# Kernel tuning notes

Hardware: AMD Instinct MI355X
Metric: run time of the kernel (lower is better)

The kernel has to match this reference:

```python
import jax, jax.numpy as jnp
import numpy as np


def setup_inputs() -> dict:
    key = jax.random.key(0)
    ks = jax.random.split(key, 8)
    B, L, E, U = 32, 2048, 1024, 1024
    s = 0.02
    return {
        "dec_hidden": jax.random.normal(ks[0], (B, E), jnp.float32),
        "enc_output": jax.random.normal(ks[1], (B, L, E), jnp.float32),
        "prev_coverage": jax.random.uniform(ks[2], (B, L, 1), jnp.float32),
        "Ws_k": jax.random.normal(ks[3], (E, U), jnp.float32) * s,
        "Ws_b": jnp.zeros((U,), jnp.float32),
        "Wh_k": jax.random.normal(ks[4], (E, U), jnp.float32) * s,
        "Wh_b": jnp.zeros((U,), jnp.float32),
        "Wc_k": jax.random.normal(ks[5], (1, U), jnp.float32) * s,
        "Wc_b": jnp.zeros((U,), jnp.float32),
        "V_k": jax.random.normal(ks[6], (U, 1), jnp.float32) * s,
        "V_b": jnp.zeros((1,), jnp.float32),
        "enc_pad_mask": jnp.ones((B, L), jnp.int32),
        "use_coverage": 1,
    }


def reference(dec_hidden, enc_output, prev_coverage, Ws_k, Ws_b, Wh_k, Wh_b,
              Wc_k, Wc_b, V_k, V_b, enc_pad_mask, use_coverage):
    # projections: [B,L,U] + [B,1,U] (+ [B,L,U] coverage term)
    pre = jnp.einsum('ble,eu->blu', enc_output, Ws_k) + Ws_b \
        + (dec_hidden @ Wh_k + Wh_b)[:, None, :]
    if use_coverage:
        pre = pre + (prev_coverage @ Wc_k + Wc_b)
    score = jnp.tanh(pre) @ V_k + V_b              # [B, L, 1]
    mask = enc_pad_mask.astype(score.dtype)        # [B, L]
    masked_score = (score[..., 0] * mask)[..., None]  # [B, L, 1]
    attention_weights = jax.nn.softmax(masked_score, axis=1)
    coverage = attention_weights + prev_coverage if use_coverage else attention_weights
    context_vector = jnp.sum(attention_weights * enc_output, axis=1)  # [B, E]
    return (context_vector, attention_weights, coverage)
```

## Files before the change

kernel.cpp:

```cpp
#include <hip/hip_runtime.h>
#include <hip/hip_bf16.h>
#include <math.h>

typedef float f32x4 __attribute__((ext_vector_type(4)));
typedef short short8 __attribute__((ext_vector_type(8)));
typedef unsigned short u16x8 __attribute__((ext_vector_type(8)));

static __device__ __forceinline__ unsigned short f2bf(float f) {
    unsigned u = __builtin_bit_cast(unsigned, f);
    unsigned r = (u + 0x7FFFu + ((u >> 16) & 1u)) >> 16;
    return (unsigned short)r;
}
static __device__ __forceinline__ float bf2f(unsigned short h) {
    unsigned u = ((unsigned)h) << 16;
    return __builtin_bit_cast(float, u);
}
static __device__ __forceinline__ float fast_tanh(float x) {
    float ax = fminf(fmaxf(x, -9.f), 9.f);
    float e = __expf(2.f * ax);
    return 1.f - 2.f / (e + 1.f);
}

#define GLD16(g, l) __builtin_amdgcn_global_load_lds(                        \
    (const __attribute__((address_space(1))) void*)(g),                      \
    (__attribute__((address_space(3))) void*)(l), 16, 0, 0)

__global__ __launch_bounds__(256) void prep_kernel(
    const float* __restrict__ enc, unsigned short* __restrict__ encB,
    const float* __restrict__ ws, unsigned short* __restrict__ wst,
    const float* __restrict__ dh, const float* __restrict__ whk,
    float* __restrict__ base_part)
{
    __shared__ unsigned short tile[64][65];
    __shared__ float dS[128];
    const int bid = blockIdx.x, tid = threadIdx.x;

    if (bid < 16384) {
        const size_t base0 = (size_t)bid * 4096;
#pragma unroll
        for (int i = 0; i < 4; i++) {
            size_t g = base0 + (size_t)i * 1024 + tid * 4;
            f32x4 v = *(const f32x4*)(enc + g);
            ushort4 w;
            w.x = f2bf(v.x); w.y = f2bf(v.y); w.z = f2bf(v.z); w.w = f2bf(v.w);
            *(ushort4*)(encB + g) = w;
        }
    } else if (bid < 16640) {
        const int b2 = bid - 16384;
        const int e0 = (b2 & 15) * 64, u0 = (b2 >> 4) * 64;
#pragma unroll
        for (int i = 0; i < 16; i++) {
            int idx = i * 256 + tid;
            int r = idx >> 6, c = idx & 63;
            tile[r][c] = f2bf(ws[(size_t)(e0 + r) * 1024 + u0 + c]);
        }
        __syncthreads();
#pragma unroll
        for (int i = 0; i < 16; i++) {
            int idx = i * 256 + tid;
            int r = idx >> 6, c = idx & 63;
            wst[(size_t)(u0 + r) * 1024 + e0 + c] = tile[c][r];
        }
    } else {
        const int b3 = bid - 16640;
        const int b = b3 & 31, ec = b3 >> 5;
        const int e0 = ec * 128;
        if (tid < 128) dS[tid] = dh[b * 1024 + e0 + tid];
        __syncthreads();
        f32x4 acc = {0.f, 0.f, 0.f, 0.f};
#pragma unroll 4
        for (int e = 0; e < 128; e++)
            acc += dS[e] * *(const f32x4*)(whk + (size_t)(e0 + e) * 1024 + tid * 4);
        *(f32x4*)(base_part + (size_t)ec * 32768 + b * 1024 + tid * 4) = acc;
    }
}

#define BARRM() asm volatile("s_barrier" ::: "memory")
#define PRIO1() __builtin_amdgcn_s_setprio(1)
#define PRIO0() __builtin_amdgcn_s_setprio(0)
#define VMC6()  asm volatile("s_waitcnt vmcnt(6)" ::: "memory")
#define VMC4()  asm volatile("s_waitcnt vmcnt(4)" ::: "memory")
#define VMC0()  asm volatile("s_waitcnt vmcnt(0)" ::: "memory")

__global__ __launch_bounds__(512, 2) void score_gemm_8ph(
    const unsigned short* __restrict__ encB,
    const unsigned short* __restrict__ wst,
    const float* __restrict__ base_part,
    const float* __restrict__ cov,
    const float* __restrict__ wc,
    const float* __restrict__ vk,
    const float* __restrict__ wsb, const float* __restrict__ whb,
    const float* __restrict__ wcb,
    const int* __restrict__ ucov,
    float* __restrict__ score_part)
{
    __shared__ __align__(16) unsigned short As[2][16384];
    __shared__ __align__(16) unsigned short Bs[2][16384];

    const int tid = threadIdx.x;
    const int bid = blockIdx.x;
    const int sidx = bid >> 3;
    const int row_blk = (bid & 7) * 32 + (sidx >> 2);
    const int u_blk = sidx & 3;
    const int row0 = row_blk << 8;
    const int u0 = u_blk << 8;

    const int lane = tid & 63;
    const int wid  = tid >> 6;
    const int wm = wid >> 2, wn = wid & 3;
    const int l16 = lane & 15, quad = lane >> 4;

    const int k8 = (lane & 7) ^ (lane >> 3);
    unsigned offA[2][2], offB[2][2];
    int dstA[2][2], dstB[2][2];
#pragma unroll
    for (int g = 0; g < 2; g++) {
        const int uu = wid * 2 + g;
#pragma unroll
        for (int h = 0; h < 2; h++) {
            const int ra = ((uu & 8) << 4) + (h << 6) + ((uu & 7) << 3);
            const int rb = ((uu >> 2) << 6) + (h << 5) + ((uu & 3) << 3);
            dstA[g][h] = ra * 64 + lane * 8;
            dstB[g][h] = rb * 64 + lane * 8;
            offA[g][h] = (unsigned)(row0 + ra + (lane >> 3)) * 1024u + (unsigned)(k8 * 8);
            offB[g][h] = (unsigned)(u0 + rb + (lane >> 3)) * 1024u + (unsigned)(k8 * 8);
        }
    }

    const int aBase = (wm * 128 + l16) * 64;
    const int bBase = (wn * 64 + l16) * 64;
    const int ch0 = ((quad) ^ (l16 & 7)) * 8;
    const int ch1 = ((4 + quad) ^ (l16 & 7)) * 8;

#define STAGE_A(bf, h, kt) do {                                             \
    GLD16(encB + offA[0][h] + ((kt) << 6), &As[bf][dstA[0][h]]);            \
    GLD16(encB + offA[1][h] + ((kt) << 6), &As[bf][dstA[1][h]]); } while (0)
#define STAGE_B(bf, h, kt) do {                                             \
    GLD16(wst + offB[0][h] + ((kt) << 6), &Bs[bf][dstB[0][h]]);             \
    GLD16(wst + offB[1][h] + ((kt) << 6), &Bs[bf][dstB[1][h]]); } while (0)

    f32x4 acc[8][4] = {};
    short8 aF[4][2], bF0[2][2], bF1[2][2];

#define LOAD_AF(bf, r) do {                                                 \
    _Pragma("unroll")                                                       \
    for (int fi = 0; fi < 4; fi++) {                                        \
        aF[fi][0] = *(const short8*)&As[bf][aBase + (r)*4096 + fi*1024 + ch0]; \
        aF[fi][1] = *(const short8*)&As[bf][aBase + (r)*4096 + fi*1024 + ch1]; \
    } } while (0)
#define LOAD_BF(bf, c, BF) do {                                             \
    _Pragma("unroll")                                                       \
    for (int fj = 0; fj < 2; fj++) {                                        \
        BF[fj][0] = *(const short8*)&Bs[bf][bBase + (c)*2048 + fj*1024 + ch0]; \
        BF[fj][1] = *(const short8*)&Bs[bf][bBase + (c)*2048 + fj*1024 + ch1]; \
    } } while (0)
#define MFMA16(r, c, BF) do {                                               \
    _Pragma("unroll")                                                       \
    for (int ks = 0; ks < 2; ks++)                                          \
    _Pragma("unroll")                                                       \
    for (int fi = 0; fi < 4; fi++)                                          \
    _Pragma("unroll")                                                       \
    for (int fj = 0; fj < 2; fj++)                                          \
        acc[(r)*4+fi][(c)*2+fj] = __builtin_amdgcn_mfma_f32_16x16x32_bf16(  \
            aF[fi][ks], BF[fj][ks], acc[(r)*4+fi][(c)*2+fj], 0, 0, 0);      \
    } while (0)

    STAGE_A(0, 0, 0);
    STAGE_B(0, 0, 0);
    STAGE_B(0, 1, 0);
    STAGE_A(0, 1, 0);
    STAGE_A(1, 0, 1);
    STAGE_B(1, 0, 1);
    STAGE_B(1, 1, 1);
    VMC6();
    BARRM();

#pragma unroll 1
    for (int i = 0; i < 7; i++) {
        const int t1 = 2 * i + 1, t2 = 2 * i + 2, t3 = 2 * i + 3;
        LOAD_AF(0, 0); LOAD_BF(0, 0, bF0); LOAD_BF(0, 1, bF1);
        STAGE_A(1, 1, t1);
        PRIO1(); MFMA16(0, 0, bF0); MFMA16(0, 1, bF1); PRIO0();
        BARRM();
        LOAD_AF(0, 1);
        STAGE_A(0, 0, t2); STAGE_B(0, 0, t2);
        PRIO1(); MFMA16(1, 0, bF0); MFMA16(1, 1, bF1); PRIO0();
        VMC4();
        BARRM();
        LOAD_AF(1, 0); LOAD_BF(1, 0, bF0); LOAD_BF(1, 1, bF1);
        STAGE_B(0, 1, t2); STAGE_A(0, 1, t2);
        PRIO1(); MFMA16(0, 0, bF0); MFMA16(0, 1, bF1); PRIO0();
        BARRM();
        LOAD_AF(1, 1);
        STAGE_A(1, 0, t3); STAGE_B(1, 0, t3); STAGE_B(1, 1, t3);
        PRIO1(); MFMA16(1, 0, bF0); MFMA16(1, 1, bF1); PRIO0();
        VMC6();
        BARRM();
    }

    LOAD_AF(0, 0); LOAD_BF(0, 0, bF0); LOAD_BF(0, 1, bF1);
    STAGE_A(1, 1, 15);
    PRIO1(); MFMA16(0, 0, bF0); MFMA16(0, 1, bF1); PRIO0();
    BARRM();
    LOAD_AF(0, 1);
    PRIO1(); MFMA16(1, 0, bF0); MFMA16(1, 1, bF1); PRIO0();
    VMC0();
    BARRM();
    LOAD_AF(1, 0); LOAD_BF(1, 0, bF0); LOAD_BF(1, 1, bF1);
    PRIO1(); MFMA16(0, 0, bF0); MFMA16(0, 1, bF1); PRIO0();
    BARRM();
    LOAD_AF(1, 1);
    PRIO1(); MFMA16(1, 0, bF0); MFMA16(1, 1, bF1); PRIO0();

    const int use_cov = *ucov;
    const int b = row0 >> 11;
    float baseR[4], wcR[4], vvR[4];
#pragma unroll
    for (int cf = 0; cf < 4; cf++) {
        int u = u0 + wn * 64 + cf * 16 + l16;
        float s = wsb[u] + whb[u] + (use_cov ? wcb[u] : 0.f);
#pragma unroll
        for (int p = 0; p < 8; p++) s += base_part[p * 32768 + b * 1024 + u];
        baseR[cf] = s;
        wcR[cf] = use_cov ? wc[u] : 0.f;
        vvR[cf] = vk[u];
    }
    float* sred = (float*)&Bs[0][0];
#pragma unroll
    for (int rf = 0; rf < 8; rf++) {
        float part[4] = {0.f, 0.f, 0.f, 0.f};
#pragma unroll
        for (int j = 0; j < 4; j++) {
            int rl = wm * 128 + rf * 16 + quad * 4 + j;
            float cvv = use_cov ? cov[row0 + rl] : 0.f;
#pragma unroll
            for (int cf = 0; cf < 4; cf++) {
                float pre = acc[rf][cf][j] + baseR[cf] + cvv * wcR[cf];
                part[j] += fast_tanh(pre) * vvR[cf];
            }
        }
#pragma unroll
        for (int j = 0; j < 4; j++) {
            float v = part[j];
            v += __shfl_xor(v, 1);
            v += __shfl_xor(v, 2);
            v += __shfl_xor(v, 4);
            v += __shfl_xor(v, 8);
            if (l16 == 0) sred[wn * 256 + wm * 128 + rf * 16 + quad * 4 + j] = v;
        }
    }
    __syncthreads();
    if (tid < 256)
        score_part[(size_t)u_blk * 65536 + row0 + tid] =
            sred[tid] + sred[256 + tid] + sred[512 + tid] + sred[768 + tid];

#undef STAGE_A
#undef STAGE_B
#undef LOAD_AF
#undef LOAD_BF
#undef MFMA16
}

__global__ __launch_bounds__(1024) void softmax_kernel(
    const float* __restrict__ score_part, int nplanes,
    const float* __restrict__ vb,
    const int* __restrict__ mask, const float* __restrict__ cov,
    const int* __restrict__ ucov,
    float* __restrict__ attn_out, float* __restrict__ cov_out)
{
    __shared__ float redA[16], redB[16];
    __shared__ float bc0, bc1;
    const int b = blockIdx.x, tid = threadIdx.x;
    const int i0 = b * 2048 + tid, i1 = i0 + 1024;
    const float vbv = vb[0];
    const int uc = *ucov;

    float s0 = 0.f, s1 = 0.f;
    for (int p = 0; p < nplanes; p++) {
        s0 += score_part[(size_t)p * 65536 + i0];
        s1 += score_part[(size_t)p * 65536 + i1];
    }
    s0 = (s0 + vbv) * (float)mask[i0];
    s1 = (s1 + vbv) * (float)mask[i1];

    float m = fmaxf(s0, s1);
#pragma unroll
    for (int off = 1; off < 64; off <<= 1) m = fmaxf(m, __shfl_xor(m, off));
    if ((tid & 63) == 0) redA[tid >> 6] = m;
    __syncthreads();
    if (tid < 16) {
        float v = redA[tid];
#pragma unroll
        for (int off = 1; off < 16; off <<= 1) v = fmaxf(v, __shfl_xor(v, off));
        if (tid == 0) bc0 = v;
    }
    __syncthreads();
    const float M = bc0;

    float e0 = __expf(s0 - M), e1 = __expf(s1 - M);
    float s = e0 + e1;
#pragma unroll
    for (int off = 1; off < 64; off <<= 1) s += __shfl_xor(s, off);
    if ((tid & 63) == 0) redB[tid >> 6] = s;
    __syncthreads();
    if (tid < 16) {
        float v = redB[tid];
#pragma unroll
        for (int off = 1; off < 16; off <<= 1) v += __shfl_xor(v, off);
        if (tid == 0) bc1 = v;
    }
    __syncthreads();
    const float inv = 1.f / bc1;

    float a0 = e0 * inv, a1 = e1 * inv;
    attn_out[i0] = a0;
    attn_out[i1] = a1;
    cov_out[i0] = a0 + (uc ? cov[i0] : 0.f);
    cov_out[i1] = a1 + (uc ? cov[i1] : 0.f);
}

__global__ __launch_bounds__(256) void context_bf16(const unsigned short* __restrict__ encB,
                                                    const float* __restrict__ attn,
                                                    float* __restrict__ out_ctx) {
    __shared__ float aS[2048];
    __shared__ float red[4][64];
    const int b = blockIdx.x, ec = blockIdx.y, tid = threadIdx.x;
    const int e0 = ec * 64;
    for (int i = tid; i < 2048; i += 256) aS[i] = attn[b * 2048 + i];
    __syncthreads();
    const int es = (tid & 7) * 8;
    const int lo = tid >> 3;
    float acc[8] = {};
    for (int l = lo; l < 2048; l += 32) {
        u16x8 w = *(const u16x8*)(encB + (size_t)(b * 2048 + l) * 1024 + e0 + es);
        float a = aS[l];
#pragma unroll
        for (int j = 0; j < 8; j++) acc[j] = fmaf(a, bf2f(w[j]), acc[j]);
    }
#pragma unroll
    for (int j = 0; j < 8; j++) {
        float v = acc[j];
        v += __shfl_xor(v, 8);
        v += __shfl_xor(v, 16);
        v += __shfl_xor(v, 32);
        acc[j] = v;
    }
    const int wv = tid >> 6;
    if ((tid & 63) < 8) {
#pragma unroll
        for (int j = 0; j < 8; j++) red[wv][(tid & 7) * 8 + j] = acc[j];
    }
    __syncthreads();
    if (tid < 64)
        out_ctx[b * 1024 + e0 + tid] = red[0][tid] + red[1][tid] + red[2][tid] + red[3][tid];
}

#define BM 128
#define BN 128
#define BK 32
#define LDT 40
__global__ __launch_bounds__(256) void score_gemm_f32(
    const float* __restrict__ enc, const unsigned short* __restrict__ wst,
    const float* __restrict__ base_part, const float* __restrict__ cov,
    const float* __restrict__ wc, const float* __restrict__ vk,
    const float* __restrict__ wsb, const float* __restrict__ whb,
    const float* __restrict__ wcb,
    const int* __restrict__ ucov, float* __restrict__ score)
{
    __shared__ unsigned short As[BM * LDT];
    __shared__ unsigned short Bs[BN * LDT];
    __shared__ float covS[BM];
    __shared__ float baseS[BN], wcS[BN], vvS[BN];
    const int tid = threadIdx.x;
    const int row0 = blockIdx.x * BM, u0 = blockIdx.y * BN;
    const int b = row0 >> 11;
    const int use_cov = *ucov;
    if (tid < BM) covS[tid] = use_cov ? cov[row0 + tid] : 0.f;
    if (tid < BN) {
        int u = u0 + tid;
        float s = wsb[u] + whb[u] + (use_cov ? wcb[u] : 0.f);
#pragma unroll
        for (int p = 0; p < 8; p++) s += base_part[p * 32768 + b * 1024 + u];
        baseS[tid] = s;
        wcS[tid] = use_cov ? wc[u] : 0.f;
        vvS[tid] = vk[u];
    }
    const int lane = tid & 63, wid = tid >> 6;
    const int wm = wid >> 1, wn = wid & 1;
    const int l16 = lane & 15, quad = lane >> 4;
    f32x4 acc[4][4] = {};
    for (int k0 = 0; k0 < 1024; k0 += BK) {
        __syncthreads();
#pragma unroll
        for (int i = 0; i < 4; i++) {
            int f = i * 256 + tid;
            int r = f >> 3, c4 = f & 7;
            const float* p = enc + (size_t)(row0 + r) * 1024 + k0 + c4 * 4;
            ushort4 w;
            w.x = f2bf(p[0]); w.y = f2bf(p[1]); w.z = f2bf(p[2]); w.w = f2bf(p[3]);
            *(ushort4*)&As[r * LDT + c4 * 4] = w;
        }
#pragma unroll
        for (int i = 0; i < 2; i++) {
            int f = i * 256 + tid;
            int r = f >> 2, c8 = f & 3;
            uint4 w = *(const uint4*)(wst + (size_t)(u0 + r) * 1024 + k0 + c8 * 8);
            *(uint4*)&Bs[r * LDT + c8 * 8] = w;
        }
        __syncthreads();
        short8 a[4], bb[4];
#pragma unroll
        for (int t = 0; t < 4; t++) {
            a[t]  = *(const short8*)&As[(wm * 64 + t * 16 + l16) * LDT + quad * 8];
            bb[t] = *(const short8*)&Bs[(wn * 64 + t * 16 + l16) * LDT + quad * 8];
        }
#pragma unroll
        for (int i = 0; i < 4; i++)
#pragma unroll
            for (int j = 0; j < 4; j++)
                acc[i][j] = __builtin_amdgcn_mfma_f32_16x16x32_bf16(a[i], bb[j], acc[i][j], 0, 0, 0);
    }
#pragma unroll
    for (int i = 0; i < 4; i++) {
        float part[4] = {0.f, 0.f, 0.f, 0.f};
#pragma unroll
        for (int r = 0; r < 4; r++) {
            float cv = covS[wm * 64 + i * 16 + quad * 4 + r];
#pragma unroll
            for (int j = 0; j < 4; j++) {
                int ul = wn * 64 + j * 16 + l16;
                part[r] += fast_tanh(acc[i][j][r] + baseS[ul] + cv * wcS[ul]) * vvS[ul];
            }
        }
#pragma unroll
        for (int r = 0; r < 4; r++) {
            float v = part[r];
            v += __shfl_xor(v, 1);
            v += __shfl_xor(v, 2);
            v += __shfl_xor(v, 4);
            v += __shfl_xor(v, 8);
            if (l16 == 0)
                atomicAdd(&score[row0 + wm * 64 + i * 16 + quad * 4 + r], v);
        }
    }
}

__global__ __launch_bounds__(256) void context_f32(const float* __restrict__ enc,
                                                   const float* __restrict__ attn,
                                                   float* __restrict__ ctx) {
    __shared__ float aS[128];
    const int b = blockIdx.x, lc = blockIdx.y, tid = threadIdx.x;
    const int l0 = lc * 128;
    if (tid < 128) aS[tid] = attn[b * 2048 + l0 + tid];
    __syncthreads();
    const float* p = enc + ((size_t)(b * 2048 + l0)) * 1024 + tid * 4;
    f32x4 acc = {0.f, 0.f, 0.f, 0.f};
#pragma unroll 4
    for (int l = 0; l < 128; l++) acc += *(const f32x4*)(p + (size_t)l * 1024) * aS[l];
    float* o = ctx + b * 1024 + tid * 4;
    atomicAdd(o + 0, acc.x);
    atomicAdd(o + 1, acc.y);
    atomicAdd(o + 2, acc.z);
    atomicAdd(o + 3, acc.w);
}

__global__ __launch_bounds__(256) void prep2_kernel(
    const float* __restrict__ ws, unsigned short* __restrict__ wst,
    const float* __restrict__ dh, const float* __restrict__ whk,
    float* __restrict__ base_part)
{
    __shared__ unsigned short tile[64][65];
    __shared__ float dS[128];
    const int bid = blockIdx.x, tid = threadIdx.x;
    if (bid < 256) {
        const int e0 = (bid & 15) * 64, u0 = (bid >> 4) * 64;
#pragma unroll
        for (int i = 0; i < 16; i++) {
            int idx = i * 256 + tid;
            int r = idx >> 6, c = idx & 63;
            tile[r][c] = f2bf(ws[(size_t)(e0 + r) * 1024 + u0 + c]);
        }
        __syncthreads();
#pragma unroll
        for (int i = 0; i < 16; i++) {
            int idx = i * 256 + tid;
            int r = idx >> 6, c = idx & 63;
            wst[(size_t)(u0 + r) * 1024 + e0 + c] = tile[c][r];
        }
    } else {
        const int b3 = bid - 256;
        const int b = b3 & 31, ec = b3 >> 5;
        const int e0 = ec * 128;
        if (tid < 128) dS[tid] = dh[b * 1024 + e0 + tid];
        __syncthreads();
        f32x4 acc = {0.f, 0.f, 0.f, 0.f};
#pragma unroll 4
        for (int e = 0; e < 128; e++)
            acc += dS[e] * *(const f32x4*)(whk + (size_t)(e0 + e) * 1024 + tid * 4);
        *(f32x4*)(base_part + (size_t)ec * 32768 + b * 1024 + tid * 4) = acc;
    }
}

extern "C" void kernel_launch(void* const* d_in, const int* in_sizes, int n_in,
                              void* d_out, int out_size, void* d_ws, size_t ws_size,
                              hipStream_t stream) {
    const float* dec_hidden = (const float*)d_in[0];
    const float* enc        = (const float*)d_in[1];
    const float* prev_cov   = (const float*)d_in[2];
    const float* Ws_k       = (const float*)d_in[3];
    const float* Ws_b       = (const float*)d_in[4];
    const float* Wh_k       = (const float*)d_in[5];
    const float* Wh_b       = (const float*)d_in[6];
    const float* Wc_k       = (const float*)d_in[7];
    const float* Wc_b       = (const float*)d_in[8];
    const float* V_k        = (const float*)d_in[9];
    const float* V_b        = (const float*)d_in[10];
    const int*   mask       = (const int*)d_in[11];
    const int*   ucov       = (const int*)d_in[12];

    float* out_ctx  = (float*)d_out;
    float* out_attn = out_ctx + 32 * 1024;
    float* out_cov  = out_attn + 65536;

    char* ws = (char*)d_ws;
    unsigned short* wst = (unsigned short*)ws;
    float* base_part  = (float*)(ws + 2097152);
    float* score_part = (float*)(ws + 3145728);
    unsigned short* encB = (unsigned short*)(ws + 5242880);
    const size_t need_fast = 5242880 + (size_t)32 * 2048 * 1024 * 2;

    if (ws_size >= need_fast) {
        prep_kernel<<<16896, 256, 0, stream>>>(enc, encB, Ws_k, wst, dec_hidden, Wh_k, base_part);
        score_gemm_8ph<<<dim3(1024), dim3(512), 0, stream>>>(
            encB, wst, base_part, prev_cov, Wc_k, V_k, Ws_b, Wh_b, Wc_b, ucov, score_part);
        softmax_kernel<<<32, 1024, 0, stream>>>(score_part, 4, V_b, mask, prev_cov, ucov, out_attn, out_cov);
        context_bf16<<<dim3(32, 16), 256, 0, stream>>>(encB, out_attn, out_ctx);
    } else {
        hipMemsetAsync(score_part, 0, 65536 * sizeof(float), stream);
        hipMemsetAsync(out_ctx, 0, 32 * 1024 * sizeof(float), stream);
        prep2_kernel<<<512, 256, 0, stream>>>(Ws_k, wst, dec_hidden, Wh_k, base_part);
        score_gemm_f32<<<dim3(512, 8), 256, 0, stream>>>(
            enc, wst, base_part, prev_cov, Wc_k, V_k, Ws_b, Wh_b, Wc_b, ucov, score_part);
        softmax_kernel<<<32, 1024, 0, stream>>>(score_part, 1, V_b, mask, prev_cov, ucov, out_attn, out_cov);
        context_f32<<<dim3(32, 16), 256, 0, stream>>>(enc, out_attn, out_ctx);
    }
}
```

Measured before the change: 592.5 us.

## Prefetch LDS fragments one phase ahead in score GEMM and fuse softmax into context

Restructures the 8-phase MFMA GEMM loop so the A and B fragments for the next phase are read from LDS while the current phase's MFMAs run. It uses double-buffered register fragments (aFA/aFB, bfE/bfO), loads B once per k-tile, and adjusts the vmcnt waits to match. Separately, it drops the standalone softmax launch and has each context block recompute the softmax over the score planes. That removes one kernel launch and the attention round-trip through global memory, at the cost of 16x redundant softmax work per batch row and more register pressure in the GEMM.

```diff
diff --git a/kernel.cpp b/kernel.cpp
--- a/kernel.cpp
+++ b/kernel.cpp
@@ -78,7 +78,7 @@
 #define BARRM() asm volatile("s_barrier" ::: "memory")
 #define PRIO1() __builtin_amdgcn_s_setprio(1)
 #define PRIO0() __builtin_amdgcn_s_setprio(0)
-#define VMC6()  asm volatile("s_waitcnt vmcnt(6)" ::: "memory")
+#define VMC8()  asm volatile("s_waitcnt vmcnt(8)" ::: "memory")
 #define VMC4()  asm volatile("s_waitcnt vmcnt(4)" ::: "memory")
 #define VMC0()  asm volatile("s_waitcnt vmcnt(0)" ::: "memory")
 
@@ -140,77 +140,76 @@
     GLD16(wst + offB[1][h] + ((kt) << 6), &Bs[bf][dstB[1][h]]); } while (0)
 
     f32x4 acc[8][4] = {};
-    short8 aF[4][2], bF0[2][2], bF1[2][2];
-
-#define LOAD_AF(bf, r) do {                                                 \
+    short8 aFA[4][2], aFB[4][2];
+    short8 bfE[2][2][2], bfO[2][2][2];
+
+#define LOAD_A(bf, r, DST) do {                                             \
     _Pragma("unroll")                                                       \
     for (int fi = 0; fi < 4; fi++) {                                        \
-        aF[fi][0] = *(const short8*)&As[bf][aBase + (r)*4096 + fi*1024 + ch0]; \
-        aF[fi][1] = *(const short8*)&As[bf][aBase + (r)*4096 + fi*1024 + ch1]; \
+        DST[fi][0] = *(const short8*)&As[bf][aBase + (r)*4096 + fi*1024 + ch0]; \
+        DST[fi][1] = *(const short8*)&As[bf][aBase + (r)*4096 + fi*1024 + ch1]; \
     } } while (0)
-#define LOAD_BF(bf, c, BF) do {                                             \
+#define LOAD_B(bf, DST) do {                                                \
+    _Pragma("unroll")                                                       \
+    for (int c = 0; c < 2; c++)                                             \
     _Pragma("unroll")                                                       \
     for (int fj = 0; fj < 2; fj++) {                                        \
-        BF[fj][0] = *(const short8*)&Bs[bf][bBase + (c)*2048 + fj*1024 + ch0]; \
-        BF[fj][1] = *(const short8*)&Bs[bf][bBase + (c)*2048 + fj*1024 + ch1]; \
+        DST[c][fj][0] = *(const short8*)&Bs[bf][bBase + c*2048 + fj*1024 + ch0]; \
+        DST[c][fj][1] = *(const short8*)&Bs[bf][bBase + c*2048 + fj*1024 + ch1]; \
     } } while (0)
-#define MFMA16(r, c, BF) do {                                               \
+#define MFMA_ROW(r, AF, BF) do {                                            \
     _Pragma("unroll")                                                       \
     for (int ks = 0; ks < 2; ks++)                                          \
     _Pragma("unroll")                                                       \
     for (int fi = 0; fi < 4; fi++)                                          \
     _Pragma("unroll")                                                       \
+    for (int c = 0; c < 2; c++)                                             \
+    _Pragma("unroll")                                                       \
     for (int fj = 0; fj < 2; fj++)                                          \
-        acc[(r)*4+fi][(c)*2+fj] = __builtin_amdgcn_mfma_f32_16x16x32_bf16(  \
-            aF[fi][ks], BF[fj][ks], acc[(r)*4+fi][(c)*2+fj], 0, 0, 0);      \
+        acc[(r)*4+fi][c*2+fj] = __builtin_amdgcn_mfma_f32_16x16x32_bf16(    \
+            AF[fi][ks], BF[c][fj][ks], acc[(r)*4+fi][c*2+fj], 0, 0, 0);     \
     } while (0)
 
-    STAGE_A(0, 0, 0);
-    STAGE_B(0, 0, 0);
-    STAGE_B(0, 1, 0);
-    STAGE_A(0, 1, 0);
-    STAGE_A(1, 0, 1);
-    STAGE_B(1, 0, 1);
-    STAGE_B(1, 1, 1);
-    VMC6();
+    STAGE_A(0, 0, 0); STAGE_B(0, 0, 0); STAGE_B(0, 1, 0); STAGE_A(0, 1, 0);
+    STAGE_A(1, 0, 1); STAGE_B(1, 0, 1); STAGE_B(1, 1, 1); STAGE_A(1, 1, 1);
+    VMC8();
     BARRM();
+    LOAD_A(0, 0, aFA); LOAD_B(0, bfE);
 
 #pragma unroll 1
     for (int i = 0; i < 7; i++) {
-        const int t1 = 2 * i + 1, t2 = 2 * i + 2, t3 = 2 * i + 3;
-        LOAD_AF(0, 0); LOAD_BF(0, 0, bF0); LOAD_BF(0, 1, bF1);
-        STAGE_A(1, 1, t1);
-        PRIO1(); MFMA16(0, 0, bF0); MFMA16(0, 1, bF1); PRIO0();
-        BARRM();
-        LOAD_AF(0, 1);
+        const int t2 = 2 * i + 2, t3 = 2 * i + 3;
+        LOAD_A(0, 1, aFB);
         STAGE_A(0, 0, t2); STAGE_B(0, 0, t2);
-        PRIO1(); MFMA16(1, 0, bF0); MFMA16(1, 1, bF1); PRIO0();
+        PRIO1(); MFMA_ROW(0, aFA, bfE); PRIO0();
         VMC4();
         BARRM();
-        LOAD_AF(1, 0); LOAD_BF(1, 0, bF0); LOAD_BF(1, 1, bF1);
+        LOAD_A(1, 0, aFA); LOAD_B(1, bfO);
         STAGE_B(0, 1, t2); STAGE_A(0, 1, t2);
-        PRIO1(); MFMA16(0, 0, bF0); MFMA16(0, 1, bF1); PRIO0();
+        PRIO1(); MFMA_ROW(1, aFB, bfE); PRIO0();
         BARRM();
-        LOAD_AF(1, 1);
-        STAGE_A(1, 0, t3); STAGE_B(1, 0, t3); STAGE_B(1, 1, t3);
-        PRIO1(); MFMA16(1, 0, bF0); MFMA16(1, 1, bF1); PRIO0();
-        VMC6();
+        LOAD_A(1, 1, aFB);
+        STAGE_A(1, 0, t3); STAGE_B(1, 0, t3);
+        PRIO1(); MFMA_ROW(0, aFA, bfO); PRIO0();
+        VMC4();
         BARRM();
-    }
-
-    LOAD_AF(0, 0); LOAD_BF(0, 0, bF0); LOAD_BF(0, 1, bF1);
-    STAGE_A(1, 1, 15);
-    PRIO1(); MFMA16(0, 0, bF0); MFMA16(0, 1, bF1); PRIO0();
-    BARRM();
-    LOAD_AF(0, 1);
-    PRIO1(); MFMA16(1, 0, bF0); MFMA16(1, 1, bF1); PRIO0();
+        LOAD_A(0, 0, aFA); LOAD_B(0, bfE);
+        STAGE_B(1, 1, t3); STAGE_A(1, 1, t3);
+        PRIO1(); MFMA_ROW(1, aFB, bfO); PRIO0();
+        BARRM();
+    }
+
+    LOAD_A(0, 1, aFB);
+    PRIO1(); MFMA_ROW(0, aFA, bfE); PRIO0();
     VMC0();
     BARRM();
-    LOAD_AF(1, 0); LOAD_BF(1, 0, bF0); LOAD_BF(1, 1, bF1);
-    PRIO1(); MFMA16(0, 0, bF0); MFMA16(0, 1, bF1); PRIO0();
+    LOAD_A(1, 0, aFA); LOAD_B(1, bfO);
+    PRIO1(); MFMA_ROW(1, aFB, bfE); PRIO0();
     BARRM();
-    LOAD_AF(1, 1);
-    PRIO1(); MFMA16(1, 0, bF0); MFMA16(1, 1, bF1); PRIO0();
+    LOAD_A(1, 1, aFB);
+    PRIO1(); MFMA_ROW(0, aFA, bfO); PRIO0();
+    BARRM();
+    PRIO1(); MFMA_ROW(1, aFB, bfO); PRIO0();
 
     const int use_cov = *ucov;
     const int b = row0 >> 11;
@@ -256,9 +255,102 @@
 
 #undef STAGE_A
 #undef STAGE_B
-#undef LOAD_AF
-#undef LOAD_BF
-#undef MFMA16
+#undef LOAD_A
+#undef LOAD_B
+#undef MFMA_ROW
+}
+
+__global__ __launch_bounds__(256) void context_fused(
+    const unsigned short* __restrict__ encB,
+    const float* __restrict__ score_part, int nplanes,
+    const float* __restrict__ vb,
+    const int* __restrict__ mask, const float* __restrict__ cov,
+    const int* __restrict__ ucov,
+    float* __restrict__ attn_out, float* __restrict__ cov_out,
+    float* __restrict__ out_ctx)
+{
+    __shared__ float aS[2048];
+    __shared__ float red[4][64];
+    __shared__ float redM[4], redS[4];
+    const int b = blockIdx.x, ec = blockIdx.y, tid = threadIdx.x;
+    const int e0 = ec * 64;
+    const int wv = tid >> 6;
+    const float vbv = vb[0];
+    const int uc = *ucov;
+
+    const int l0 = tid * 8;
+    float sv[8] = {0.f, 0.f, 0.f, 0.f, 0.f, 0.f, 0.f, 0.f};
+    for (int p = 0; p < nplanes; p++) {
+        const float* sp = score_part + (size_t)p * 65536 + b * 2048 + l0;
+        f32x4 v0 = *(const f32x4*)sp;
+        f32x4 v1 = *(const f32x4*)(sp + 4);
+        sv[0] += v0.x; sv[1] += v0.y; sv[2] += v0.z; sv[3] += v0.w;
+        sv[4] += v1.x; sv[5] += v1.y; sv[6] += v1.z; sv[7] += v1.w;
+    }
+    int4 mk0 = *(const int4*)(mask + b * 2048 + l0);
+    int4 mk1 = *(const int4*)(mask + b * 2048 + l0 + 4);
+    sv[0] = (sv[0] + vbv) * (float)mk0.x;
+    sv[1] = (sv[1] + vbv) * (float)mk0.y;
+    sv[2] = (sv[2] + vbv) * (float)mk0.z;
+    sv[3] = (sv[3] + vbv) * (float)mk0.w;
+    sv[4] = (sv[4] + vbv) * (float)mk1.x;
+    sv[5] = (sv[5] + vbv) * (float)mk1.y;
+    sv[6] = (sv[6] + vbv) * (float)mk1.z;
+    sv[7] = (sv[7] + vbv) * (float)mk1.w;
+
+    float m = sv[0];
+#pragma unroll
+    for (int j = 1; j < 8; j++) m = fmaxf(m, sv[j]);
+#pragma unroll
+    for (int off = 1; off < 64; off <<= 1) m = fmaxf(m, __shfl_xor(m, off));
+    if ((tid & 63) == 0) redM[wv] = m;
+    __syncthreads();
+    const float M = fmaxf(fmaxf(redM[0], redM[1]), fmaxf(redM[2], redM[3]));
+
+    float e[8], s = 0.f;
+#pragma unroll
+    for (int j = 0; j < 8; j++) { e[j] = __expf(sv[j] - M); s += e[j]; }
+#pragma unroll
+    for (int off = 1; off < 64; off <<= 1) s += __shfl_xor(s, off);
+    if ((tid & 63) == 0) redS[wv] = s;
+    __syncthreads();
+    const float inv = 1.f / (redS[0] + redS[1] + redS[2] + redS[3]);
+
+#pragma unroll
+    for (int j = 0; j < 8; j++) {
+        float a = e[j] * inv;
+        aS[l0 + j] = a;
+        if (ec == 0) {
+            attn_out[b * 2048 + l0 + j] = a;
+            cov_out[b * 2048 + l0 + j] = a + (uc ? cov[b * 2048 + l0 + j] : 0.f);
+        }
+    }
+    __syncthreads();
+
+    const int es = (tid & 7) * 8;
+    const int lo = tid >> 3;
+    float acc[8] = {};
+    for (int l = lo; l < 2048; l += 32) {
+        u16x8 w = *(const u16x8*)(encB + (size_t)(b * 2048 + l) * 1024 + e0 + es);
+        float a = aS[l];
+#pragma unroll
+        for (int j = 0; j < 8; j++) acc[j] = fmaf(a, bf2f(w[j]), acc[j]);
+    }
+#pragma unroll
+    for (int j = 0; j < 8; j++) {
+        float v = acc[j];
+        v += __shfl_xor(v, 8);
+        v += __shfl_xor(v, 16);
+        v += __shfl_xor(v, 32);
+        acc[j] = v;
+    }
+    if ((tid & 63) < 8) {
+#pragma unroll
+        for (int j = 0; j < 8; j++) red[wv][(tid & 7) * 8 + j] = acc[j];
+    }
+    __syncthreads();
+    if (tid < 64)
+        out_ctx[b * 1024 + e0 + tid] = red[0][tid] + red[1][tid] + red[2][tid] + red[3][tid];
 }
 
 __global__ __launch_bounds__(1024) void softmax_kernel(
@@ -317,42 +409,6 @@
     attn_out[i1] = a1;
     cov_out[i0] = a0 + (uc ? cov[i0] : 0.f);
     cov_out[i1] = a1 + (uc ? cov[i1] : 0.f);
-}
-
-__global__ __launch_bounds__(256) void context_bf16(const unsigned short* __restrict__ encB,
-                                                    const float* __restrict__ attn,
-                                                    float* __restrict__ out_ctx) {
-    __shared__ float aS[2048];
-    __shared__ float red[4][64];
-    const int b = blockIdx.x, ec = blockIdx.y, tid = threadIdx.x;
-    const int e0 = ec * 64;
-    for (int i = tid; i < 2048; i += 256) aS[i] = attn[b * 2048 + i];
-    __syncthreads();
-    const int es = (tid & 7) * 8;
-    const int lo = tid >> 3;
-    float acc[8] = {};
-    for (int l = lo; l < 2048; l += 32) {
-        u16x8 w = *(const u16x8*)(encB + (size_t)(b * 2048 + l) * 1024 + e0 + es);
-        float a = aS[l];
-#pragma unroll
-        for (int j = 0; j < 8; j++) acc[j] = fmaf(a, bf2f(w[j]), acc[j]);
-    }
-#pragma unroll
-    for (int j = 0; j < 8; j++) {
-        float v = acc[j];
-        v += __shfl_xor(v, 8);
-        v += __shfl_xor(v, 16);
-        v += __shfl_xor(v, 32);
-        acc[j] = v;
-    }
-    const int wv = tid >> 6;
-    if ((tid & 63) < 8) {
-#pragma unroll
-        for (int j = 0; j < 8; j++) red[wv][(tid & 7) * 8 + j] = acc[j];
-    }
-    __syncthreads();
-    if (tid < 64)
-        out_ctx[b * 1024 + e0 + tid] = red[0][tid] + red[1][tid] + red[2][tid] + red[3][tid];
 }
 
 #define BM 128
@@ -533,8 +589,8 @@
         prep_kernel<<<16896, 256, 0, stream>>>(enc, encB, Ws_k, wst, dec_hidden, Wh_k, base_part);
         score_gemm_8ph<<<dim3(1024), dim3(512), 0, stream>>>(
             encB, wst, base_part, prev_cov, Wc_k, V_k, Ws_b, Wh_b, Wc_b, ucov, score_part);
-        softmax_kernel<<<32, 1024, 0, stream>>>(score_part, 4, V_b, mask, prev_cov, ucov, out_attn, out_cov);
-        context_bf16<<<dim3(32, 16), 256, 0, stream>>>(encB, out_attn, out_ctx);
+        context_fused<<<dim3(32, 16), 256, 0, stream>>>(
+            encB, score_part, 4, V_b, mask, prev_cov, ucov, out_attn, out_cov, out_ctx);
     } else {
         hipMemsetAsync(score_part, 0, 65536 * sizeof(float), stream);
         hipMemsetAsync(out_ctx, 0, 32 * 1024 * sizeof(float), stream);
```

After: 1.144 ms. 93.1% more time.

## Fuse softmax into context kernel and widen nontemporal bf16 conversion loads

Applied to the files above, without the earlier changes.

The separate softmax launch is removed. Each of the 16 context blocks per batch now recomputes the softmax over its batch row redundantly, and only the ec==0 blocks write attention and coverage. The context kernel goes from 256 to 512 threads. The enc fp32-to-bf16 conversion in prep now handles 8 elements per thread with nontemporal loads and 16-byte stores. The intent is to save a launch and a global round trip for the attention weights, at the cost of recomputing the softmax 16 times.

```diff
diff --git a/kernel.cpp b/kernel.cpp
--- a/kernel.cpp
+++ b/kernel.cpp
@@ -38,12 +38,14 @@
     if (bid < 16384) {
         const size_t base0 = (size_t)bid * 4096;
 #pragma unroll
-        for (int i = 0; i < 4; i++) {
-            size_t g = base0 + (size_t)i * 1024 + tid * 4;
-            f32x4 v = *(const f32x4*)(enc + g);
-            ushort4 w;
-            w.x = f2bf(v.x); w.y = f2bf(v.y); w.z = f2bf(v.z); w.w = f2bf(v.w);
-            *(ushort4*)(encB + g) = w;
+        for (int i = 0; i < 2; i++) {
+            size_t g = base0 + (size_t)i * 2048 + tid * 8;
+            f32x4 v0 = __builtin_nontemporal_load((const f32x4*)(enc + g));
+            f32x4 v1 = __builtin_nontemporal_load((const f32x4*)(enc + g) + 1);
+            u16x8 w;
+            w[0] = f2bf(v0.x); w[1] = f2bf(v0.y); w[2] = f2bf(v0.z); w[3] = f2bf(v0.w);
+            w[4] = f2bf(v1.x); w[5] = f2bf(v1.y); w[6] = f2bf(v1.z); w[7] = f2bf(v1.w);
+            *(u16x8*)(encB + g) = w;
         }
     } else if (bid < 16640) {
         const int b2 = bid - 16384;
@@ -261,6 +263,98 @@
 #undef MFMA16
 }
 
+__global__ __launch_bounds__(512) void context_fused(
+    const unsigned short* __restrict__ encB,
+    const float* __restrict__ score_part, int nplanes,
+    const float* __restrict__ vb,
+    const int* __restrict__ mask, const float* __restrict__ cov,
+    const int* __restrict__ ucov,
+    float* __restrict__ attn_out, float* __restrict__ cov_out,
+    float* __restrict__ out_ctx)
+{
+    __shared__ float aS[2048];
+    __shared__ float red[8][64];
+    __shared__ float redM[8], redS[8];
+    const int b = blockIdx.x, ec = blockIdx.y, tid = threadIdx.x;
+    const int e0 = ec * 64;
+    const int wv = tid >> 6;
+    const float vbv = vb[0];
+    const int uc = *ucov;
+
+    const int l0 = tid * 4;
+    float sv[4] = {0.f, 0.f, 0.f, 0.f};
+    for (int p = 0; p < nplanes; p++) {
+        f32x4 v0 = *(const f32x4*)(score_part + (size_t)p * 65536 + b * 2048 + l0);
+        sv[0] += v0.x; sv[1] += v0.y; sv[2] += v0.z; sv[3] += v0.w;
+    }
+    int4 mk = *(const int4*)(mask + b * 2048 + l0);
+    sv[0] = (sv[0] + vbv) * (float)mk.x;
+    sv[1] = (sv[1] + vbv) * (float)mk.y;
+    sv[2] = (sv[2] + vbv) * (float)mk.z;
+    sv[3] = (sv[3] + vbv) * (float)mk.w;
+
+    float m = fmaxf(fmaxf(sv[0], sv[1]), fmaxf(sv[2], sv[3]));
+#pragma unroll
+    for (int off = 1; off < 64; off <<= 1) m = fmaxf(m, __shfl_xor(m, off));
+    if ((tid & 63) == 0) redM[wv] = m;
+    __syncthreads();
+    float M = redM[0];
+#pragma unroll
+    for (int w = 1; w < 8; w++) M = fmaxf(M, redM[w]);
+
+    float e[4], s = 0.f;
+#pragma unroll
+    for (int j = 0; j < 4; j++) { e[j] = __expf(sv[j] - M); s += e[j]; }
+#pragma unroll
+    for (int off = 1; off < 64; off <<= 1) s += __shfl_xor(s, off);
+    if ((tid & 63) == 0) redS[wv] = s;
+    __syncthreads();
+    float den = redS[0];
+#pragma unroll
+    for (int w = 1; w < 8; w++) den += redS[w];
+    const float inv = 1.f / den;
+
+#pragma unroll
+    for (int j = 0; j < 4; j++) {
+        float a = e[j] * inv;
+        aS[l0 + j] = a;
+        if (ec == 0) {
+            attn_out[b * 2048 + l0 + j] = a;
+            cov_out[b * 2048 + l0 + j] = a + (uc ? cov[b * 2048 + l0 + j] : 0.f);
+        }
+    }
+    __syncthreads();
+
+    const int es = (tid & 7) * 8;
+    const int lo = tid >> 3;
+    float acc[8] = {};
+    for (int l = lo; l < 2048; l += 64) {
+        u16x8 w = *(const u16x8*)(encB + (size_t)(b * 2048 + l) * 1024 + e0 + es);
+        float a = aS[l];
+#pragma unroll
+        for (int j = 0; j < 8; j++) acc[j] = fmaf(a, bf2f(w[j]), acc[j]);
+    }
+#pragma unroll
+    for (int j = 0; j < 8; j++) {
+        float v = acc[j];
+        v += __shfl_xor(v, 8);
+        v += __shfl_xor(v, 16);
+        v += __shfl_xor(v, 32);
+        acc[j] = v;
+    }
+    if ((tid & 63) < 8) {
+#pragma unroll
+        for (int j = 0; j < 8; j++) red[wv][(tid & 7) * 8 + j] = acc[j];
+    }
+    __syncthreads();
+    if (tid < 64) {
+        float v = 0.f;
+#pragma unroll
+        for (int w = 0; w < 8; w++) v += red[w][tid];
+        out_ctx[b * 1024 + e0 + tid] = v;
+    }
+}
+
 __global__ __launch_bounds__(1024) void softmax_kernel(
     const float* __restrict__ score_part, int nplanes,
     const float* __restrict__ vb,
@@ -317,42 +411,6 @@
     attn_out[i1] = a1;
     cov_out[i0] = a0 + (uc ? cov[i0] : 0.f);
     cov_out[i1] = a1 + (uc ? cov[i1] : 0.f);
-}
-
-__global__ __launch_bounds__(256) void context_bf16(const unsigned short* __restrict__ encB,
-                                                    const float* __restrict__ attn,
-                                                    float* __restrict__ out_ctx) {
-    __shared__ float aS[2048];
-    __shared__ float red[4][64];
-    const int b = blockIdx.x, ec = blockIdx.y, tid = threadIdx.x;
-    const int e0 = ec * 64;
-    for (int i = tid; i < 2048; i += 256) aS[i] = attn[b * 2048 + i];
-    __syncthreads();
-    const int es = (tid & 7) * 8;
-    const int lo = tid >> 3;
-    float acc[8] = {};
-    for (int l = lo; l < 2048; l += 32) {
-        u16x8 w = *(const u16x8*)(encB + (size_t)(b * 2048 + l) * 1024 + e0 + es);
-        float a = aS[l];
-#pragma unroll
-        for (int j = 0; j < 8; j++) acc[j] = fmaf(a, bf2f(w[j]), acc[j]);
-    }
-#pragma unroll
-    for (int j = 0; j < 8; j++) {
-        float v = acc[j];
-        v += __shfl_xor(v, 8);
-        v += __shfl_xor(v, 16);
-        v += __shfl_xor(v, 32);
-        acc[j] = v;
-    }
-    const int wv = tid >> 6;
-    if ((tid & 63) < 8) {
-#pragma unroll
-        for (int j = 0; j < 8; j++) red[wv][(tid & 7) * 8 + j] = acc[j];
-    }
-    __syncthreads();
-    if (tid < 64)
-        out_ctx[b * 1024 + e0 + tid] = red[0][tid] + red[1][tid] + red[2][tid] + red[3][tid];
 }
 
 #define BM 128
@@ -533,8 +591,8 @@
         prep_kernel<<<16896, 256, 0, stream>>>(enc, encB, Ws_k, wst, dec_hidden, Wh_k, base_part);
         score_gemm_8ph<<<dim3(1024), dim3(512), 0, stream>>>(
             encB, wst, base_part, prev_cov, Wc_k, V_k, Ws_b, Wh_b, Wc_b, ucov, score_part);
-        softmax_kernel<<<32, 1024, 0, stream>>>(score_part, 4, V_b, mask, prev_cov, ucov, out_attn, out_cov);
-        context_bf16<<<dim3(32, 16), 256, 0, stream>>>(encB, out_attn, out_ctx);
+        context_fused<<<dim3(32, 16), 512, 0, stream>>>(
+            encB, score_part, 4, V_b, mask, prev_cov, ucov, out_attn, out_cov, out_ctx);
     } else {
         hipMemsetAsync(score_part, 0, 65536 * sizeof(float), stream);
         hipMemsetAsync(out_ctx, 0, 32 * 1024 * sizeof(float), stream);
```

Result: faster. 569.3 us (-3.9%).
